# Kernel tuning notes

Hardware: AMD Instinct MI355X
Metric: run time of the kernel (lower is better)

## Reference

```python
import jax, jax.numpy as jnp
import numpy as np
from jax import lax

B, N, C = 8, 16384, 96
ROPE_BASE = 10000.0


def _rope(x):
    """Faithful port of the module's RoPE. x: (b, h, w, c).
    Note: the original computes angles over the h axis but, due to torch
    broadcasting of (h, k_max) against (b, h, w, k_max), the rotation is
    applied along the w axis (valid since h == w)."""
    b, h, w, c = x.shape
    k_max = c // 2
    theta = 1.0 / (ROPE_BASE ** (jnp.arange(k_max, dtype=x.dtype) / k_max))  # (k_max,)
    angles = jnp.arange(h, dtype=x.dtype)[:, None] * theta                  # (h, k_max)
    cos = jnp.cos(angles)[None, None, :, :]  # broadcast over w axis
    sin = jnp.sin(angles)[None, None, :, :]
    xr = x.reshape(b, h, w, k_max, 2)
    xre, xim = xr[..., 0], xr[..., 1]
    ore = xre * cos - xim * sin
    oim = xre * sin + xim * cos
    return jnp.stack([ore, oim], axis=-1).reshape(b, h, w, c)


def setup_inputs() -> dict:
    key = jax.random.key(0)
    ks = jax.random.split(key, 5)
    return {
        "x": jax.random.normal(ks[0], (B, N, C), dtype=jnp.float32),
        "qk_w": jax.random.normal(ks[1], (2 * C, C), dtype=jnp.float32) * 0.05,
        "qk_b": jax.random.normal(ks[2], (2 * C,), dtype=jnp.float32) * 0.02,
        "lepe_w": jax.random.normal(ks[3], (C, 1, 3, 3), dtype=jnp.float32) * 0.1,
        "lepe_b": jax.random.normal(ks[4], (C,), dtype=jnp.float32) * 0.02,
        "num_heads": 4,
    }


def reference(x, qk_w, qk_b, lepe_w, lepe_b, num_heads):
    b, n, c = x.shape
    h = w = int(round(n ** 0.5))
    d = c // num_heads
    inv_sqrt_n = float(n) ** (-0.5)

    qk = x @ qk_w.T + qk_b                        # (b, n, 2c)
    q = jax.nn.elu(qk[..., :c]) + 1.0             # (b, n, c)
    k = jax.nn.elu(qk[..., c:]) + 1.0
    v = x

    q_rope = _rope(q.reshape(b, h, w, c)).reshape(b, n, num_heads, d).transpose(0, 2, 1, 3)
    k_rope = _rope(k.reshape(b, h, w, c)).reshape(b, n, num_heads, d).transpose(0, 2, 1, 3)
    qh = q.reshape(b, n, num_heads, d).transpose(0, 2, 1, 3)  # (b, H, n, d)
    kh = k.reshape(b, n, num_heads, d).transpose(0, 2, 1, 3)
    vh = v.reshape(b, n, num_heads, d).transpose(0, 2, 1, 3)

    k_mean = kh.mean(axis=2, keepdims=True)                         # (b, H, 1, d)
    z = 1.0 / (jnp.einsum('bhnd,bhmd->bhnm', qh, k_mean) + 1e-6)    # (b, H, n, 1)
    kv = jnp.einsum('bhnd,bhne->bhde', k_rope * inv_sqrt_n, vh * inv_sqrt_n)  # (b, H, d, d)
    out = jnp.einsum('bhnd,bhde->bhne', q_rope, kv) * z             # (b, H, n, d)
    out = out.transpose(0, 2, 1, 3).reshape(b, n, c)

    # LePE: depthwise 3x3 conv on v laid out as (b, c, h, w)
    v_img = vh.transpose(0, 2, 1, 3).reshape(b, h, w, c).transpose(0, 3, 1, 2)
    lepe = lax.conv_general_dilated(
        v_img, lepe_w, window_strides=(1, 1), padding='SAME',
        feature_group_count=c, dimension_numbers=('NCHW', 'OIHW', 'NCHW'))
    lepe = lepe + lepe_b[None, :, None, None]
    return out + lepe.transpose(0, 2, 3, 1).reshape(b, n, c)
```

## Files before the change

kernel.cpp:

```cpp
#include <hip/hip_runtime.h>


#define NLINE 16384
#define CCH 96
#define KTP 136
#define QSP 98
#define OUTP 98
#define THETA_COEF 0.2768273412406135f
#define LOG2_2PI   2.6514961294723187f

typedef __attribute__((ext_vector_type(4))) float f32x4;
typedef __attribute__((ext_vector_type(8))) short bf16x8;
typedef __attribute__((ext_vector_type(2))) __fp16 fp16x2;

__device__ __forceinline__ unsigned short f2bf(float f) {
  unsigned int u = __float_as_uint(f);
  u += 0x7FFFu + ((u >> 16) & 1u);
  return (unsigned short)(u >> 16);
}
__device__ __forceinline__ float bf2f(unsigned short h) {
  return __uint_as_float(((unsigned int)h) << 16);
}
__device__ __forceinline__ bf16x8 pack_bf8(f32x4 v0, f32x4 v1) {
  bf16x8 r;
  r[0] = (short)f2bf(v0.x); r[1] = (short)f2bf(v0.y);
  r[2] = (short)f2bf(v0.z); r[3] = (short)f2bf(v0.w);
  r[4] = (short)f2bf(v1.x); r[5] = (short)f2bf(v1.y);
  r[6] = (short)f2bf(v1.z); r[7] = (short)f2bf(v1.w);
  return r;
}

__global__ void prep_w2(const float* __restrict__ qkw,
                        unsigned short* __restrict__ wfrag,
                        float* __restrict__ kv_g) {
  int idx = blockIdx.x * 256 + threadIdx.x;
  if (idx < 19200) kv_g[idx] = 0.0f;
  if (idx < 2304) {
    int u = idx;
    int lane = u & 63;
    int nt = (u >> 6) % 6;
    int rest = u / 384;
    int kk = rest % 3, half = rest / 3;
    int lr = lane & 15, q4 = lane >> 4;
    const float* src = qkw + (half * 96 + nt * 16 + lr) * 96 + kk * 32 + q4 * 8;
    unsigned short* dst = wfrag + (size_t)u * 8;
#pragma unroll
    for (int j = 0; j < 8; ++j) dst[j] = f2bf(src[j]);
  }
}

__global__ __launch_bounds__(256, 4) void la_k1(
    const float* __restrict__ x, const unsigned short* __restrict__ wfrag,
    const float* __restrict__ qkb, float* __restrict__ kv_g,
    float* __restrict__ ksum_g)
{
  const int tid  = threadIdx.x;
  const int b    = blockIdx.x >> 7;
  const int tile = blockIdx.x & 127;

  __shared__ alignas(16) unsigned short kqt[96 * KTP];
  __shared__ float ksum_s[96];

  if (tid < 96) ksum_s[tid] = 0.0f;
  __syncthreads();

  const int wave = tid >> 6;
  const int lane = tid & 63;
  const int lr   = lane & 15;
  const int q4   = lane >> 4;
  const int row0 = wave * 32;
  const float* xb = x + ((size_t)b * NLINE + (size_t)tile * 128) * CCH;

  bf16x8 afr[2][3];
#pragma unroll
  for (int mt = 0; mt < 2; ++mt)
#pragma unroll
    for (int kk = 0; kk < 3; ++kk) {
      const float* ap = xb + (row0 + mt * 16 + lr) * CCH + kk * 32 + q4 * 8;
      afr[mt][kk] = pack_bf8(((const f32x4*)ap)[0], ((const f32x4*)ap)[1]);
    }

  float biasv[6];
#pragma unroll
  for (int nt = 0; nt < 6; ++nt) biasv[nt] = qkb[96 + nt * 16 + lr];

  f32x4 acc[2][6];
#pragma unroll
  for (int mt = 0; mt < 2; ++mt)
#pragma unroll
    for (int nt = 0; nt < 6; ++nt) acc[mt][nt] = (f32x4){0.f, 0.f, 0.f, 0.f};

#pragma unroll
  for (int kk = 0; kk < 3; ++kk) {
#pragma unroll
    for (int nt = 0; nt < 6; ++nt) {
      bf16x8 bf = *(const bf16x8*)&wfrag[(size_t)(((3 + kk) * 6 + nt) * 64 + lane) * 8];
      acc[0][nt] = __builtin_amdgcn_mfma_f32_16x16x32_bf16(afr[0][kk], bf, acc[0][nt], 0, 0, 0);
      acc[1][nt] = __builtin_amdgcn_mfma_f32_16x16x32_bf16(afr[1][kk], bf, acc[1][nt], 0, 0, 0);
    }
  }

  const int odd = lr & 1;
#pragma unroll
  for (int nt = 0; nt < 6; ++nt) {
    const int col = nt * 16 + lr;
    const float threv = exp2f(-THETA_COEF * (float)(col >> 1) - LOG2_2PI);
    float csum = 0.0f;
    float vv[2][4];
#pragma unroll
    for (int mt = 0; mt < 2; ++mt)
#pragma unroll
      for (int rg = 0; rg < 4; ++rg) {
        float v = acc[mt][nt][rg] + biasv[nt];
        v = (v > 0.0f) ? (v + 1.0f) : __expf(v);
        csum += v;
        vv[mt][rg] = v;
      }
    atomicAdd(&ksum_s[col], csum);
#pragma unroll
    for (int mt = 0; mt < 2; ++mt) {
      unsigned long long pk = 0;
#pragma unroll
      for (int rg = 0; rg < 4; ++rg) {
        float p = __shfl_xor(vv[mt][rg], 1);
        int r = row0 + mt * 16 + q4 * 4 + rg;
        float rev = (float)r * threv;
        float sn = __builtin_amdgcn_sinf(rev);
        float cn = __builtin_amdgcn_cosf(rev);
        float o = odd ? (p * sn + vv[mt][rg] * cn)
                      : (vv[mt][rg] * cn - p * sn);
        pk |= (unsigned long long)f2bf(o) << (16 * rg);
      }
      *(unsigned long long*)&kqt[col * KTP + row0 + mt * 16 + q4 * 4] = pk;
    }
  }
  __syncthreads();

  if (tid < 96) atomicAdd(&ksum_g[b * 96 + tid], ksum_s[tid]);

  const int h = wave;
  f32x4 kvacc[2][2];
#pragma unroll
  for (int mt = 0; mt < 2; ++mt)
#pragma unroll
    for (int nt = 0; nt < 2; ++nt) kvacc[mt][nt] = (f32x4){0.f, 0.f, 0.f, 0.f};

#pragma unroll
  for (int kk = 0; kk < 4; ++kk) {
    const int rbase = kk * 32 + q4 * 8;
    bf16x8 ka[2], vb[2];
#pragma unroll
    for (int mt = 0; mt < 2; ++mt) {
      int c = 24 * h + mt * 16 + lr; if (c > 95) c = 95;
      ka[mt] = *(const bf16x8*)&kqt[c * KTP + rbase];
    }
#pragma unroll
    for (int nt = 0; nt < 2; ++nt) {
      int c = 24 * h + nt * 16 + lr; if (c > 95) c = 95;
#pragma unroll
      for (int j = 0; j < 8; ++j)
        vb[nt][j] = (short)f2bf(xb[(rbase + j) * CCH + c]);
    }
#pragma unroll
    for (int mt = 0; mt < 2; ++mt)
#pragma unroll
      for (int nt = 0; nt < 2; ++nt)
        kvacc[mt][nt] = __builtin_amdgcn_mfma_f32_16x16x32_bf16(ka[mt], vb[nt], kvacc[mt][nt], 0, 0, 0);
  }

  const float inv_n = 1.0f / 16384.0f;
  float* kvb = kv_g + ((size_t)b * 4 + h) * 576;
#pragma unroll
  for (int mt = 0; mt < 2; ++mt)
#pragma unroll
    for (int rg = 0; rg < 4; ++rg) {
      int d = mt * 16 + q4 * 4 + rg;
      if (d < 24) {
#pragma unroll
        for (int nt = 0; nt < 2; ++nt) {
          int e = nt * 16 + lr;
          if (e < 24) atomicAdd(&kvb[d * 24 + e], kvacc[mt][nt][rg] * inv_n);
        }
      }
    }
}

__global__ __launch_bounds__(256, 6) void la_k2(
    const float* __restrict__ x, const unsigned short* __restrict__ wfrag,
    const float* __restrict__ qkb, const float* __restrict__ lepe_w,
    const float* __restrict__ lepe_b, const float* __restrict__ kv_g,
    const float* __restrict__ ksum_g, float* __restrict__ out)
{
  const int tid = threadIdx.x;
  const int b   = blockIdx.x & 7;
  const int seg = blockIdx.x >> 3;
  const int y   = seg >> 1;

  __shared__ alignas(16) unsigned short qs[64 * QSP];
  __shared__ float lepe_s[9 * 96];

  for (int i = tid; i < 864; i += 256) {
    int ch = i / 9, tap = i % 9;
    lepe_s[tap * 96 + (ch & 3) * 24 + (ch >> 2)] = lepe_w[i];
  }

  const int wave = tid >> 6;
  const int lane = tid & 63;
  const int lr   = lane & 15;
  const int q4   = lane >> 4;

  float biasv[6];
#pragma unroll
  for (int nt = 0; nt < 6; ++nt) biasv[nt] = qkb[nt * 16 + lr];

  const float* xb = x + ((size_t)b * NLINE + (size_t)seg * 64) * CCH;
  bf16x8 afrag[3];
#pragma unroll
  for (int kk = 0; kk < 3; ++kk) {
    const float* ap = xb + (wave * 16 + lr) * CCH + kk * 32 + q4 * 8;
    afrag[kk] = pack_bf8(((const f32x4*)ap)[0], ((const f32x4*)ap)[1]);
  }

  f32x4 acc[6];
#pragma unroll
  for (int nt = 0; nt < 6; ++nt) acc[nt] = (f32x4){0.f, 0.f, 0.f, 0.f};
#pragma unroll
  for (int kk = 0; kk < 3; ++kk) {
#pragma unroll
    for (int nt = 0; nt < 6; ++nt) {
      bf16x8 bf = *(const bf16x8*)&wfrag[(size_t)((kk * 6 + nt) * 64 + lane) * 8];
      acc[nt] = __builtin_amdgcn_mfma_f32_16x16x32_bf16(afrag[kk], bf, acc[nt], 0, 0, 0);
    }
  }
#pragma unroll
  for (int nt = 0; nt < 6; ++nt) {
    const int col = nt * 16 + lr;
#pragma unroll
    for (int rg = 0; rg < 4; ++rg) {
      int t = wave * 16 + q4 * 4 + rg;
      float v = acc[nt][rg] + biasv[nt];
      v = (v > 0.0f) ? (v + 1.0f) : __expf(v);
      qs[t * QSP + col] = f2bf(v);
    }
  }
  __syncthreads();

  float res[24];
  {
    const int t  = lane;
    const int h  = __builtin_amdgcn_readfirstlane(wave);
    const int xw = ((seg & 1) << 6) + t;
    const float inv_n = 1.0f / 16384.0f;

    float qv[24];
    const unsigned int* qrow = (const unsigned int*)&qs[t * QSP + 24 * h];
#pragma unroll
    for (int u = 0; u < 12; ++u) {
      unsigned int w = qrow[u];
      qv[2 * u]     = bf2f((unsigned short)(w & 0xFFFFu));
      qv[2 * u + 1] = bf2f((unsigned short)(w >> 16));
    }

    const float* km = ksum_g + b * 96 + 24 * h;
    float dot = 0.0f;
#pragma unroll
    for (int d2 = 0; d2 < 24; ++d2) dot += qv[d2] * km[d2];
    const float z = 1.0f / (dot * inv_n + 1e-6f);

#pragma unroll
    for (int jj = 0; jj < 12; ++jj) {
      float threv = exp2f(-THETA_COEF * (float)(12 * h + jj) - LOG2_2PI);
      float rev = (float)xw * threv;
      float sn = __builtin_amdgcn_sinf(rev);
      float cn = __builtin_amdgcn_cosf(rev);
      float re = qv[2 * jj], im = qv[2 * jj + 1];
      qv[2 * jj]     = re * cn - im * sn;
      qv[2 * jj + 1] = re * sn + im * cn;
    }

    const float* kvh = kv_g + ((size_t)b * 4 + h) * 576;
#pragma unroll
    for (int e = 0; e < 24; ++e) res[e] = 0.0f;
    for (int d2 = 0; d2 < 24; ++d2) {
      float qd = qv[d2];
#pragma unroll
      for (int e = 0; e < 24; ++e) res[e] += qd * kvh[d2 * 24 + e];
    }
    const float* lb = lepe_b + 24 * h;
#pragma unroll
    for (int e = 0; e < 24; ++e) res[e] = res[e] * z + lb[e];
  }
  __syncthreads();

  __fp16* outs = (__fp16*)qs;
  {
    const int t = lane;
    const int h = wave;
#pragma unroll
    for (int u = 0; u < 12; ++u) {
      fp16x2 pk = __builtin_amdgcn_cvt_pkrtz(res[2 * u], res[2 * u + 1]);
      *(fp16x2*)&outs[t * OUTP + 24 * h + 2 * u] = pk;
    }
  }
  __syncthreads();

  float* ob = out + ((size_t)b * NLINE + (size_t)seg * 64) * CCH;
  const float* xg = x + (size_t)b * NLINE * CCH;
#pragma unroll
  for (int k = 0; k < 6; ++k) {
    int idx = tid + 256 * k;
    int tl = idx / 24, c4 = idx % 24;
    int ch0 = c4 * 4;
    int xw = ((seg & 1) << 6) + tl;

    fp16x2 p0 = *(const fp16x2*)&outs[tl * OUTP + ch0];
    fp16x2 p1 = *(const fp16x2*)&outs[tl * OUTP + ch0 + 2];
    float r0 = (float)p0[0], r1 = (float)p0[1];
    float r2 = (float)p1[0], r3 = (float)p1[1];

#pragma unroll
    for (int dy = 0; dy < 3; ++dy) {
      int yy = y + dy - 1;
      if (yy < 0 || yy > 127) continue;
      const float* rowp = xg + ((size_t)yy * 128) * CCH;
#pragma unroll
      for (int dx = 0; dx < 3; ++dx) {
        int xx = xw + dx - 1;
        if (xx < 0 || xx > 127) continue;
        f32x4 v = *(const f32x4*)(rowp + xx * CCH + ch0);
        const float* wp = &lepe_s[(dy * 3 + dx) * 96 + c4];
        r0 += wp[0]  * v.x;
        r1 += wp[24] * v.y;
        r2 += wp[48] * v.z;
        r3 += wp[72] * v.w;
      }
    }
    f32x4 o = { r0, r1, r2, r3 };
    ((f32x4*)ob)[idx] = o;
  }
}

extern "C" void kernel_launch(void* const* d_in, const int* in_sizes, int n_in,
                              void* d_out, int out_size, void* d_ws, size_t ws_size,
                              hipStream_t stream) {
  const float* x      = (const float*)d_in[0];
  const float* qkw    = (const float*)d_in[1];
  const float* qkb    = (const float*)d_in[2];
  const float* lepe_w = (const float*)d_in[3];
  const float* lepe_b = (const float*)d_in[4];
  float* out = (float*)d_out;

  unsigned short* wfrag = (unsigned short*)d_ws;
  float* kv_g   = (float*)((char*)d_ws + 36864);
  float* ksum_g = kv_g + 18432;

  prep_w2<<<dim3(75), dim3(256), 0, stream>>>(qkw, wfrag, kv_g);
  la_k1<<<dim3(1024), dim3(256), 0, stream>>>(x, wfrag, qkb, kv_g, ksum_g);
  la_k2<<<dim3(2048), dim3(256), 0, stream>>>(x, wfrag, qkb, lepe_w, lepe_b,
                                              kv_g, ksum_g, out);
}
```

Measured before the change: 177.7 us.

## Move per-token q·kv product onto MFMA and fuse RoPE/normalizer into GEMM epilogue

The per-thread scalar 24x24 q·kv product in la_k2 becomes MFMA bf16 ops over 16-row tiles, with kv converted to bf16 fragments. RoPE rotation (using a lane shuffle for the pair partner) and the z-normalizer dot product (via shuffle reductions into a small shared array) now happen in the first GEMM's epilogue, before q is written to shared memory. QSP padding grows to 104 for 16-byte aligned fragment loads, and the occupancy hint rises from 6 to 8. The aim is to cut scalar FMA work and per-thread register pressure. The cost is lower precision for kv (bf16) and some wasted MFMA work from the zero-padded K dimension.

```diff
diff --git a/kernel.cpp b/kernel.cpp
--- a/kernel.cpp
+++ b/kernel.cpp
@@ -4,7 +4,7 @@
 #define NLINE 16384
 #define CCH 96
 #define KTP 136
-#define QSP 98
+#define QSP 104
 #define OUTP 98
 #define THETA_COEF 0.2768273412406135f
 #define LOG2_2PI   2.6514961294723187f
@@ -185,7 +185,7 @@
     }
 }
 
-__global__ __launch_bounds__(256, 6) void la_k2(
+__global__ __launch_bounds__(256, 8) void la_k2(
     const float* __restrict__ x, const unsigned short* __restrict__ wfrag,
     const float* __restrict__ qkb, const float* __restrict__ lepe_w,
     const float* __restrict__ lepe_b, const float* __restrict__ kv_g,
@@ -197,6 +197,7 @@
   const int y   = seg >> 1;
 
   __shared__ alignas(16) unsigned short qs[64 * QSP];
+  __shared__ alignas(16) float zs[64 * 4];
   __shared__ float lepe_s[9 * 96];
 
   for (int i = tid; i < 864; i += 256) {
@@ -209,9 +210,12 @@
   const int lr   = lane & 15;
   const int q4   = lane >> 4;
 
-  float biasv[6];
-#pragma unroll
-  for (int nt = 0; nt < 6; ++nt) biasv[nt] = qkb[nt * 16 + lr];
+  float biasv[6], kmv[6];
+#pragma unroll
+  for (int nt = 0; nt < 6; ++nt) {
+    biasv[nt] = qkb[nt * 16 + lr];
+    kmv[nt]   = ksum_g[b * 96 + nt * 16 + lr];
+  }
 
   const float* xb = x + ((size_t)b * NLINE + (size_t)seg * 64) * CCH;
   bf16x8 afrag[3];
@@ -232,75 +236,116 @@
       acc[nt] = __builtin_amdgcn_mfma_f32_16x16x32_bf16(afrag[kk], bf, acc[nt], 0, 0, 0);
     }
   }
+
+  const int odd = lr & 1;
+  const int t0  = wave * 16 + q4 * 4;
+  const int xwb = ((seg & 1) << 6) + t0;
+  float d0[4], d1[4], d2[4], d3[4];
+#pragma unroll
+  for (int rg = 0; rg < 4; ++rg) { d0[rg] = 0.f; d1[rg] = 0.f; d2[rg] = 0.f; d3[rg] = 0.f; }
+
 #pragma unroll
   for (int nt = 0; nt < 6; ++nt) {
     const int col = nt * 16 + lr;
+    const float threv = exp2f(-THETA_COEF * (float)(col >> 1) - LOG2_2PI);
+    float vv[4];
 #pragma unroll
     for (int rg = 0; rg < 4; ++rg) {
-      int t = wave * 16 + q4 * 4 + rg;
       float v = acc[nt][rg] + biasv[nt];
       v = (v > 0.0f) ? (v + 1.0f) : __expf(v);
-      qs[t * QSP + col] = f2bf(v);
-    }
-  }
-  __syncthreads();
-
-  float res[24];
-  {
-    const int t  = lane;
-    const int h  = __builtin_amdgcn_readfirstlane(wave);
-    const int xw = ((seg & 1) << 6) + t;
-    const float inv_n = 1.0f / 16384.0f;
-
-    float qv[24];
-    const unsigned int* qrow = (const unsigned int*)&qs[t * QSP + 24 * h];
-#pragma unroll
-    for (int u = 0; u < 12; ++u) {
-      unsigned int w = qrow[u];
-      qv[2 * u]     = bf2f((unsigned short)(w & 0xFFFFu));
-      qv[2 * u + 1] = bf2f((unsigned short)(w >> 16));
-    }
-
-    const float* km = ksum_g + b * 96 + 24 * h;
-    float dot = 0.0f;
-#pragma unroll
-    for (int d2 = 0; d2 < 24; ++d2) dot += qv[d2] * km[d2];
-    const float z = 1.0f / (dot * inv_n + 1e-6f);
-
-#pragma unroll
-    for (int jj = 0; jj < 12; ++jj) {
-      float threv = exp2f(-THETA_COEF * (float)(12 * h + jj) - LOG2_2PI);
-      float rev = (float)xw * threv;
+      vv[rg] = v;
+    }
+#pragma unroll
+    for (int rg = 0; rg < 4; ++rg) {
+      float p = vv[rg] * kmv[nt];
+      if (nt == 0)      d0[rg] += p;
+      else if (nt == 1) { if (lr < 8) d0[rg] += p; else d1[rg] += p; }
+      else if (nt == 2) d1[rg] += p;
+      else if (nt == 3) d2[rg] += p;
+      else if (nt == 4) { if (lr < 8) d2[rg] += p; else d3[rg] += p; }
+      else              d3[rg] += p;
+    }
+#pragma unroll
+    for (int rg = 0; rg < 4; ++rg) {
+      float p = __shfl_xor(vv[rg], 1);
+      float rev = (float)(xwb + rg) * threv;
       float sn = __builtin_amdgcn_sinf(rev);
       float cn = __builtin_amdgcn_cosf(rev);
-      float re = qv[2 * jj], im = qv[2 * jj + 1];
-      qv[2 * jj]     = re * cn - im * sn;
-      qv[2 * jj + 1] = re * sn + im * cn;
-    }
-
-    const float* kvh = kv_g + ((size_t)b * 4 + h) * 576;
-#pragma unroll
-    for (int e = 0; e < 24; ++e) res[e] = 0.0f;
-    for (int d2 = 0; d2 < 24; ++d2) {
-      float qd = qv[d2];
-#pragma unroll
-      for (int e = 0; e < 24; ++e) res[e] += qd * kvh[d2 * 24 + e];
-    }
-    const float* lb = lepe_b + 24 * h;
-#pragma unroll
-    for (int e = 0; e < 24; ++e) res[e] = res[e] * z + lb[e];
-  }
+      float o = odd ? (p * sn + vv[rg] * cn)
+                    : (vv[rg] * cn - p * sn);
+      qs[(t0 + rg) * QSP + col] = f2bf(o);
+    }
+  }
+
+  {
+    const float inv_n = 1.0f / 16384.0f;
+#pragma unroll
+    for (int rg = 0; rg < 4; ++rg) {
+      float s0 = d0[rg], s1 = d1[rg], s2 = d2[rg], s3 = d3[rg];
+#pragma unroll
+      for (int m = 1; m <= 8; m <<= 1) {
+        s0 += __shfl_xor(s0, m);
+        s1 += __shfl_xor(s1, m);
+        s2 += __shfl_xor(s2, m);
+        s3 += __shfl_xor(s3, m);
+      }
+      if (lr == 0) {
+        f32x4 zv = { 1.0f / (s0 * inv_n + 1e-6f), 1.0f / (s1 * inv_n + 1e-6f),
+                     1.0f / (s2 * inv_n + 1e-6f), 1.0f / (s3 * inv_n + 1e-6f) };
+        *(f32x4*)&zs[(t0 + rg) * 4] = zv;
+      }
+    }
+  }
+  __syncthreads();
+
+  const int h2 = wave;
+  bf16x8 qa[4];
+#pragma unroll
+  for (int m = 0; m < 4; ++m) {
+    qa[m] = *(const bf16x8*)&qs[(16 * m + lr) * QSP + 24 * h2 + q4 * 8];
+    if (q4 == 3) {
+#pragma unroll
+      for (int j = 0; j < 8; ++j) qa[m][j] = 0;
+    }
+  }
+  bf16x8 kb[2];
+  {
+    const float* kvh = kv_g + ((size_t)b * 4 + h2) * 576;
+#pragma unroll
+    for (int n = 0; n < 2; ++n)
+#pragma unroll
+      for (int j = 0; j < 8; ++j) {
+        int d = q4 * 8 + j, e = n * 16 + lr;
+        kb[n][j] = (d < 24 && e < 24) ? (short)f2bf(kvh[d * 24 + e]) : (short)0;
+      }
+  }
+  f32x4 c2[4][2];
+#pragma unroll
+  for (int m = 0; m < 4; ++m)
+#pragma unroll
+    for (int n = 0; n < 2; ++n) c2[m][n] = (f32x4){0.f, 0.f, 0.f, 0.f};
+#pragma unroll
+  for (int m = 0; m < 4; ++m)
+#pragma unroll
+    for (int n = 0; n < 2; ++n)
+      c2[m][n] = __builtin_amdgcn_mfma_f32_16x16x32_bf16(qa[m], kb[n], c2[m][n], 0, 0, 0);
+
   __syncthreads();
 
   __fp16* outs = (__fp16*)qs;
   {
-    const int t = lane;
-    const int h = wave;
-#pragma unroll
-    for (int u = 0; u < 12; ++u) {
-      fp16x2 pk = __builtin_amdgcn_cvt_pkrtz(res[2 * u], res[2 * u + 1]);
-      *(fp16x2*)&outs[t * OUTP + 24 * h + 2 * u] = pk;
-    }
+    float lb0 = lepe_b[24 * h2 + lr];
+    float lb1 = (lr < 8) ? lepe_b[24 * h2 + 16 + lr] : 0.0f;
+#pragma unroll
+    for (int m = 0; m < 4; ++m)
+#pragma unroll
+      for (int rg = 0; rg < 4; ++rg) {
+        int t = 16 * m + q4 * 4 + rg;
+        float zv = zs[t * 4 + h2];
+        outs[t * OUTP + 24 * h2 + lr] = (__fp16)(c2[m][0][rg] * zv + lb0);
+        if (lr < 8)
+          outs[t * OUTP + 24 * h2 + 16 + lr] = (__fp16)(c2[m][1][rg] * zv + lb1);
+      }
   }
   __syncthreads();
 
```

After: 175.5 us. No clear change (-1.3%).
